# Performance work log

Measured on AMD Instinct MI355X. Metric: run time of the kernel, lower is better.

Reference implementation:

```python
import jax, jax.numpy as jnp
import numpy as np


def setup_inputs() -> dict:
    key = jax.random.key(0)
    ks = jax.random.split(key, 8)
    B, Cin, H, W = 4, 256, 64, 64
    Ck = Cin // 2            # 128, KAN in/out dim
    NC = 21                  # num_classes
    return {
        "x": jax.random.normal(ks[0], (B, Cin, H, W), dtype=jnp.float32),
        "conv1_w": jax.random.normal(ks[1], (Ck, Cin, 3, 3), dtype=jnp.float32) * 0.02,
        "conv1_b": jnp.zeros((Ck,), dtype=jnp.float32),
        "kan_scale": jnp.ones((Ck, Ck), dtype=jnp.float32)
                     + 0.1 * jax.random.normal(ks[2], (Ck, Ck), dtype=jnp.float32),
        "kan_translation": 0.1 * jax.random.normal(ks[3], (Ck, Ck), dtype=jnp.float32),
        "kan_wavelet_weight": jax.random.normal(ks[4], (Ck, Ck), dtype=jnp.float32) * 0.1,
        "kan_base_weight": jax.random.normal(ks[5], (Ck, Ck), dtype=jnp.float32) * 0.05,
        "conv2_w": jax.random.normal(ks[6], (NC, Ck, 1, 1), dtype=jnp.float32) * 0.05,
        "conv2_b": jnp.zeros((NC,), dtype=jnp.float32),
    }


def _conv2d(x, w, b, pad):
    y = jax.lax.conv_general_dilated(
        x, w, window_strides=(1, 1), padding=pad,
        dimension_numbers=("NCHW", "OIHW", "NCHW"))
    return y + b[None, :, None, None]


def _wavelet_kan(x, scale, translation, wav_w, base_w):
    # x: (N, Cin). Wav-KAN (DoG) layer:
    #   u = (x - translation) / scale, per (out, in) pair -> (N, O, I)
    #   dog(u) = -u * exp(-u^2 / 2)
    #   wavelet_out[n, o] = sum_i dog(u)[n, o, i] * wav_w[o, i]
    #   base_out = silu(x) @ base_w.T
    u = (x[:, None, :] - translation[None]) / scale[None]          # (N, O, I)
    dog = -u * jnp.exp(-0.5 * u * u)                               # (N, O, I)
    wav_out = jnp.einsum("noi,oi->no", dog, wav_w)                 # (N, O)
    base_out = jnp.einsum("ni,oi->no", jax.nn.silu(x), base_w)     # (N, O)
    return wav_out + base_out


def reference(x, conv1_w, conv1_b, kan_scale, kan_translation,
              kan_wavelet_weight, kan_base_weight, conv2_w, conv2_b):
    h = jax.nn.relu(_conv2d(x, conv1_w, conv1_b, ((1, 1), (1, 1))))   # (B, Ck, H, W)
    B, C, H, W = h.shape
    flat = h.transpose(0, 2, 3, 1).reshape(B * H * W, C)              # (N, Ck)
    k = _wavelet_kan(flat, kan_scale, kan_translation,
                     kan_wavelet_weight, kan_base_weight)             # (N, Ck)
    k = k.reshape(B, H, W, -1).transpose(0, 3, 1, 2)                  # (B, Ck, H, W)
    return _conv2d(k, conv2_w, conv2_b, ((0, 0), (0, 0)))             # (B, NC, H, W)
```

## Files before the change

### kernel.cpp

```cpp
#include <hip/hip_runtime.h>
#include <math.h>

typedef __attribute__((ext_vector_type(8))) short s16x8;
typedef __attribute__((ext_vector_type(4))) float f32x4;
typedef __attribute__((ext_vector_type(2))) float f32x2;

#define LOG2E 1.4426950408889634f

#define OFF_XH   0
#define OFF_WB   2097152
#define OFF_PQT  2244608
#define OFF_W2   2310144
#define OFF_H    2315520

__global__ __launch_bounds__(256) void transpose_x_k(
    const float* __restrict__ x, unsigned short* __restrict__ xh) {
  __shared__ float lsm[64][65];
  int blk = blockIdx.x;
  int pr = blk & 63, cib = (blk >> 6) & 3, bb = blk >> 8;
  int t = threadIdx.x;
  int sp0 = pr * 64;
  const float* src = x + (unsigned)(bb * 256 + cib * 64) * 4096 + sp0;
#pragma unroll
  for (int rr = 0; rr < 16; ++rr) {
    int idx = rr * 256 + t;
    int ci = idx >> 6, px = idx & 63;
    lsm[ci][px] = src[ci * 4096 + px];
  }
  __syncthreads();
#pragma unroll
  for (int rr = 0; rr < 16; ++rr) {
    int idx = rr * 256 + t;
    int px = idx >> 6, ci = idx & 63;
    unsigned u = __float_as_uint(lsm[ci][px]);
    xh[(unsigned)(bb * 4096 + sp0 + px) * 256 + cib * 64 + ci] =
        (unsigned short)((u + 0x7FFF + ((u >> 16) & 1)) >> 16);
  }
}

__global__ __launch_bounds__(256) void prep_w_k(
    const float* __restrict__ w1, const float* __restrict__ ks,
    const float* __restrict__ kt, const float* __restrict__ kw,
    const float* __restrict__ w2, float* __restrict__ ws) {
  int tid = blockIdx.x * 256 + threadIdx.x;
  unsigned short* Wb = (unsigned short*)(ws + OFF_WB);
  if (tid < 294912) {
    int j = tid & 7, co = (tid >> 3) & 63, g = (tid >> 9) & 3, r = tid >> 11;
    int t9 = r % 9, q = r / 9, ck = q & 7, chh = q >> 3;
    int ci = ck * 32 + g * 8 + j, cog = chh * 64 + co;
    unsigned u = __float_as_uint(w1[(unsigned)(cog * 256 + ci) * 9 + t9]);
    Wb[tid] = (unsigned short)((u + 0x7FFF + ((u >> 16) & 1)) >> 16);
  } else if (tid < 294912 + 16384) {
    int i2 = tid - 294912;
    int i = i2 >> 7, o = i2 & 127;
    int ic = i >> 3, k = i & 7;
    float rs = 1.f / ks[o * 128 + i];
    float T  = kt[o * 128 + i];
    float A  = -0.7213475204444817f * rs * rs;
    float Bq = -2.f * A * T;
    float C  = A * T * T;
    float P0 = -rs * kw[o * 128 + i];
    float sc = exp2f(C);
    int khi = k >> 2, klo = k & 3;
    unsigned base = ((unsigned)ic * 8 * 128 + o) * 4 + klo;
    ws[OFF_PQT + base + (0 + khi) * 512] = A;
    ws[OFF_PQT + base + (2 + khi) * 512] = Bq;
    ws[OFF_PQT + base + (4 + khi) * 512] = P0 * sc;
    ws[OFF_PQT + base + (6 + khi) * 512] = -P0 * T * sc;
  } else if (tid < 294912 + 16384 + 2688) {
    int i3 = tid - 294912 - 16384;
    int nc = i3 >> 7, k = i3 & 127;
    ws[OFF_W2 + nc * 256 + k] = w2[nc * 128 + k];
  }
}

__global__ __launch_bounds__(128) void w2b_k(
    const float* __restrict__ w2, const float* __restrict__ bw,
    float* __restrict__ w2c) {
  int nc = blockIdx.x, i = threadIdx.x;
  float acc = 0.f;
  for (int o = 0; o < 128; ++o)
    acc = fmaf(w2[nc * 128 + o], bw[o * 128 + i], acc);
  w2c[nc * 256 + 128 + i] = acc;
}

__global__ __launch_bounds__(256, 2) void conv1_mfma_k(
    const unsigned short* __restrict__ xh, const unsigned short* __restrict__ Wb,
    const float* __restrict__ b1, float* __restrict__ h) {
  __shared__ unsigned short Asm[3 * 66 * 40];
  __shared__ unsigned short Bsm[18432];
  int blk = blockIdx.x;
  int ch = blk & 1, y = (blk >> 1) & 63, bb = blk >> 7;
  int t = threadIdx.x;
  int wave = t >> 6, lane = t & 63;
  int wx = wave & 1, wn = wave >> 1;
  int l15 = lane & 15, lg = lane >> 4;

  if (t < 6) {
    int r = t >> 1, xl = (t & 1) * 65;
    float4 z = {0, 0, 0, 0};
    float4* p = (float4*)&Asm[(r * 66 + xl) * 40];
    p[0] = z; p[1] = z; p[2] = z; p[3] = z; p[4] = z;
  }

  f32x4 acc[2][2];
  f32x4 zz = {0.f, 0.f, 0.f, 0.f};
  acc[0][0] = zz; acc[0][1] = zz; acc[1][0] = zz; acc[1][1] = zz;

  int r_st = t >> 6, x_st = t & 63;
  int gy = y - 1 + r_st;
  bool arow = (r_st < 3);
  bool yok = arow & (gy >= 0) & (gy < 64);
  const unsigned short* asrc = xh + (unsigned)(bb * 4096 + gy * 64 + x_st) * 256;
  unsigned short* adst = &Asm[(r_st * 66 + x_st + 1) * 40];
  const unsigned short* bslab = Wb + ch * 8 * 18432;

  for (int ck = 0; ck < 8; ++ck) {
    float4 v0 = {0, 0, 0, 0}, v1 = v0, v2 = v0, v3 = v0;
    if (yok) {
      const float4* s = (const float4*)(asrc + ck * 32);
      v0 = s[0]; v1 = s[1]; v2 = s[2]; v3 = s[3];
    }
    if (arow) { float4* d = (float4*)adst; d[0] = v0; d[1] = v1; d[2] = v2; d[3] = v3; }
    {
      const float4* s = (const float4*)(bslab + ck * 18432);
      float4* d = (float4*)Bsm;
#pragma unroll
      for (int j = 0; j < 9; ++j) d[j * 256 + t] = s[j * 256 + t];
    }
    __syncthreads();
#pragma unroll
    for (int t9 = 0; t9 < 9; ++t9) {
      int ky = t9 / 3, kx = t9 % 3;
      s16x8 a[2], b[2];
      int abase = (ky * 66 + wx * 32 + l15 + kx) * 40 + lg * 8;
#pragma unroll
      for (int f = 0; f < 2; ++f)
        a[f] = *(const s16x8*)&Asm[abase + f * 640];
#pragma unroll
      for (int n = 0; n < 2; ++n)
        b[n] = *(const s16x8*)&Bsm[((t9 * 4 + lg) * 64 + wn * 32 + n * 16 + l15) * 8];
#pragma unroll
      for (int f = 0; f < 2; ++f)
#pragma unroll
        for (int n = 0; n < 2; ++n)
          acc[f][n] = __builtin_amdgcn_mfma_f32_16x16x32_bf16(a[f], b[n], acc[f][n], 0, 0, 0);
    }
    __syncthreads();
  }
#pragma unroll
  for (int n = 0; n < 2; ++n) {
    int co = ch * 64 + wn * 32 + n * 16 + l15;
    float bz = b1[co];
#pragma unroll
    for (int f = 0; f < 2; ++f) {
      int xbase = wx * 32 + f * 16 + lg * 4;
      float* dst = h + (unsigned)(bb * 4096 + y * 64 + xbase) * 128 + co;
#pragma unroll
      for (int r = 0; r < 4; ++r) {
        float v = acc[f][n][r] + bz;
        dst[r * 128] = v > 0.f ? v : 0.f;
      }
    }
  }
}

__global__ __launch_bounds__(512) void wavkan_k(
    const float* __restrict__ h, const float* __restrict__ PQT,
    float* __restrict__ kwout) {
  __shared__ float hsm[16][128];
  __shared__ f32x2 red[4][8][64];
  int n0 = blockIdx.x * 16;
  int t = threadIdx.x;
  {
    int row = t >> 5, c4 = (t & 31) * 4;
    *(float4*)&hsm[row][c4] = *(const float4*)&h[(unsigned)(n0 + row) * 128 + c4];
  }
  __syncthreads();

  int wave = t >> 6, lane = t & 63;
  int ich = wave & 1;
  int oh  = (wave >> 1) & 1;
  int ng  = wave >> 2;
  int w2i = wave >> 1;
  int o  = oh * 64 + lane;
  int nb = ng * 8;

  f32x2 accv[8];
#pragma unroll
  for (int n = 0; n < 8; ++n) accv[n] = (f32x2){0.f, 0.f};

  const float4* pq = (const float4*)PQT + o;

  for (int ic = ich * 8; ic < ich * 8 + 8; ++ic) {
    const float4* pp = pq + (unsigned)ic * 1024;
    float4 r0 = pp[0],   r1 = pp[128], r2 = pp[256], r3 = pp[384],
           r4 = pp[512], r5 = pp[640], r6 = pp[768], r7 = pp[896];
    f32x2 A2[4] = {{r0.x, r0.y}, {r0.z, r0.w}, {r1.x, r1.y}, {r1.z, r1.w}};
    f32x2 B2[4] = {{r2.x, r2.y}, {r2.z, r2.w}, {r3.x, r3.y}, {r3.z, r3.w}};
    f32x2 P2[4] = {{r4.x, r4.y}, {r4.z, r4.w}, {r5.x, r5.y}, {r5.z, r5.w}};
    f32x2 D2[4] = {{r6.x, r6.y}, {r6.z, r6.w}, {r7.x, r7.y}, {r7.z, r7.w}};
    int i0 = ic * 8;
#pragma unroll
    for (int n = 0; n < 8; ++n) {
      float4 h0 = *(const float4*)&hsm[nb + n][i0];
      float4 h1 = *(const float4*)&hsm[nb + n][i0 + 4];
      f32x2 hh[4] = {{h0.x, h0.y}, {h0.z, h0.w}, {h1.x, h1.y}, {h1.z, h1.w}};
      f32x2 a2 = accv[n];
#pragma unroll
      for (int q = 0; q < 4; ++q) {
        f32x2 h2 = hh[q];
        f32x2 t2 = A2[q] * h2 + B2[q];
        f32x2 u2 = t2 * h2;
        f32x2 e2;
        e2.x = __builtin_amdgcn_exp2f(u2.x);
        e2.y = __builtin_amdgcn_exp2f(u2.y);
        f32x2 v2 = P2[q] * h2 + D2[q];
        a2 = v2 * e2 + a2;
      }
      accv[n] = a2;
    }
  }

  if (ich) {
#pragma unroll
    for (int n = 0; n < 8; ++n) red[w2i][n][lane] = accv[n];
  }
  __syncthreads();
  if (!ich) {
#pragma unroll
    for (int n = 0; n < 8; ++n) {
      f32x2 r = red[w2i][n][lane];
      kwout[(unsigned)(n0 + nb + n) * 128 + o] =
          (accv[n].x + r.x) + (accv[n].y + r.y);
    }
  }
}

__global__ __launch_bounds__(256) void conv2_k(
    const float* __restrict__ kwv, const float* __restrict__ h,
    const float* __restrict__ w2c, const float* __restrict__ b2,
    float* __restrict__ out) {
  __shared__ float ksm[32][260];
  __shared__ float wsm[21 * 256];
  int n0 = blockIdx.x * 32;
  int t = threadIdx.x;
#pragma unroll 2
  for (int rr = 0; rr < 4; ++rr) {
    int idx4 = rr * 256 + t;
    int row = idx4 >> 5, c4 = (idx4 & 31) * 4;
    *(float4*)&ksm[row][c4] = *(const float4*)&kwv[(unsigned)(n0 + row) * 128 + c4];
    float4 v = *(const float4*)&h[(unsigned)(n0 + row) * 128 + c4];
    float4 s;
    s.x = v.x * __builtin_amdgcn_rcpf(1.f + __builtin_amdgcn_exp2f(-LOG2E * v.x));
    s.y = v.y * __builtin_amdgcn_rcpf(1.f + __builtin_amdgcn_exp2f(-LOG2E * v.y));
    s.z = v.z * __builtin_amdgcn_rcpf(1.f + __builtin_amdgcn_exp2f(-LOG2E * v.z));
    s.w = v.w * __builtin_amdgcn_rcpf(1.f + __builtin_amdgcn_exp2f(-LOG2E * v.w));
    *(float4*)&ksm[row][128 + c4] = s;
  }
#pragma unroll 2
  for (int j = t; j < 1344; j += 256)
    *(float4*)&wsm[j * 4] = *(const float4*)&w2c[j * 4];
  __syncthreads();

  int n = t & 31, ncg = t >> 5;
  float a0 = 0.f, a1 = 0.f, a2 = 0.f;
  bool has2 = ncg < 5;
#pragma unroll 4
  for (int i4 = 0; i4 < 64; ++i4) {
    float4 k4 = *(const float4*)&ksm[n][i4 * 4];
    float4 wA = *(const float4*)&wsm[ncg * 256 + i4 * 4];
    float4 wB = *(const float4*)&wsm[(ncg + 8) * 256 + i4 * 4];
    a0 += k4.x * wA.x + k4.y * wA.y + k4.z * wA.z + k4.w * wA.w;
    a1 += k4.x * wB.x + k4.y * wB.y + k4.z * wB.z + k4.w * wB.w;
    if (has2) {
      float4 wC = *(const float4*)&wsm[(ncg + 16) * 256 + i4 * 4];
      a2 += k4.x * wC.x + k4.y * wC.y + k4.z * wC.z + k4.w * wC.w;
    }
  }
  int gn = n0 + n, bb = gn >> 12, sp = gn & 4095;
  out[(unsigned)(bb * 21 + ncg) * 4096 + sp] = a0 + b2[ncg];
  out[(unsigned)(bb * 21 + ncg + 8) * 4096 + sp] = a1 + b2[ncg + 8];
  if (has2) out[(unsigned)(bb * 21 + ncg + 16) * 4096 + sp] = a2 + b2[ncg + 16];
}

extern "C" void kernel_launch(void* const* d_in, const int* in_sizes, int n_in,
                              void* d_out, int out_size, void* d_ws, size_t ws_size,
                              hipStream_t stream) {
  const float* x  = (const float*)d_in[0];
  const float* w1 = (const float*)d_in[1];
  const float* b1 = (const float*)d_in[2];
  const float* ks = (const float*)d_in[3];
  const float* kt = (const float*)d_in[4];
  const float* kw = (const float*)d_in[5];
  const float* kb = (const float*)d_in[6];
  const float* w2 = (const float*)d_in[7];
  const float* b2 = (const float*)d_in[8];
  float* out = (float*)d_out;
  float* ws  = (float*)d_ws;

  transpose_x_k<<<1024, 256, 0, stream>>>(x, (unsigned short*)(ws + OFF_XH));
  prep_w_k<<<1227, 256, 0, stream>>>(w1, ks, kt, kw, w2, ws);
  w2b_k<<<21, 128, 0, stream>>>(w2, kb, ws + OFF_W2);
  conv1_mfma_k<<<512, 256, 0, stream>>>((const unsigned short*)(ws + OFF_XH),
                                        (const unsigned short*)(ws + OFF_WB),
                                        b1, ws + OFF_H);
  wavkan_k<<<1024, 512, 0, stream>>>(ws + OFF_H, ws + OFF_PQT,
                                     ws + OFF_XH );
  conv2_k<<<512, 256, 0, stream>>>(ws + OFF_XH, ws + OFF_H, ws + OFF_W2, b2, out);
}
```

Measured before the change: 96.01 us.

## Stage KAN params through double-buffered LDS and drop split-K reduction in wavkan

The wavkan kernel now has each block cooperatively load every 16 KB chunk of precomputed KAN parameters into a double-buffered shared-memory tile, prefetching the next chunk into registers while computing. Before, each wave read parameters straight from global memory. The work split also changes: each wave now covers all 128 inputs for 4 rows instead of half the inputs for 8 rows, so the cross-wave reduction through shared memory goes away. The goal is less redundant global/L2 traffic for parameters, at the price of two barriers per input chunk and more LDS use.

```diff
diff --git a/kernel.cpp b/kernel.cpp
--- a/kernel.cpp
+++ b/kernel.cpp
@@ -169,40 +169,45 @@
     const float* __restrict__ h, const float* __restrict__ PQT,
     float* __restrict__ kwout) {
   __shared__ float hsm[16][128];
-  __shared__ f32x2 red[4][8][64];
+  __shared__ float4 psm[2][1024];
   int n0 = blockIdx.x * 16;
   int t = threadIdx.x;
   {
     int row = t >> 5, c4 = (t & 31) * 4;
     *(float4*)&hsm[row][c4] = *(const float4*)&h[(unsigned)(n0 + row) * 128 + c4];
   }
-  __syncthreads();
-
   int wave = t >> 6, lane = t & 63;
-  int ich = wave & 1;
-  int oh  = (wave >> 1) & 1;
-  int ng  = wave >> 2;
-  int w2i = wave >> 1;
+  int oh = wave & 1;
+  int ng = wave >> 1;
   int o  = oh * 64 + lane;
-  int nb = ng * 8;
-
-  f32x2 accv[8];
-#pragma unroll
-  for (int n = 0; n < 8; ++n) accv[n] = (f32x2){0.f, 0.f};
-
-  const float4* pq = (const float4*)PQT + o;
-
-  for (int ic = ich * 8; ic < ich * 8 + 8; ++ic) {
-    const float4* pp = pq + (unsigned)ic * 1024;
-    float4 r0 = pp[0],   r1 = pp[128], r2 = pp[256], r3 = pp[384],
-           r4 = pp[512], r5 = pp[640], r6 = pp[768], r7 = pp[896];
+  int nb = ng * 4;
+
+  f32x2 accv[4];
+#pragma unroll
+  for (int n = 0; n < 4; ++n) accv[n] = (f32x2){0.f, 0.f};
+
+  const float4* pqg = (const float4*)PQT;
+  float4 s0 = pqg[t * 2], s1 = pqg[t * 2 + 1];
+
+  for (int ic = 0; ic < 16; ++ic) {
+    int cur = ic & 1;
+    psm[cur][t * 2] = s0;
+    psm[cur][t * 2 + 1] = s1;
+    if (ic < 15) {
+      s0 = pqg[(unsigned)(ic + 1) * 1024 + t * 2];
+      s1 = pqg[(unsigned)(ic + 1) * 1024 + t * 2 + 1];
+    }
+    __syncthreads();
+    const float4* pb = &psm[cur][o];
+    float4 r0 = pb[0],   r1 = pb[128], r2 = pb[256], r3 = pb[384],
+           r4 = pb[512], r5 = pb[640], r6 = pb[768], r7 = pb[896];
     f32x2 A2[4] = {{r0.x, r0.y}, {r0.z, r0.w}, {r1.x, r1.y}, {r1.z, r1.w}};
     f32x2 B2[4] = {{r2.x, r2.y}, {r2.z, r2.w}, {r3.x, r3.y}, {r3.z, r3.w}};
     f32x2 P2[4] = {{r4.x, r4.y}, {r4.z, r4.w}, {r5.x, r5.y}, {r5.z, r5.w}};
     f32x2 D2[4] = {{r6.x, r6.y}, {r6.z, r6.w}, {r7.x, r7.y}, {r7.z, r7.w}};
     int i0 = ic * 8;
 #pragma unroll
-    for (int n = 0; n < 8; ++n) {
+    for (int n = 0; n < 4; ++n) {
       float4 h0 = *(const float4*)&hsm[nb + n][i0];
       float4 h1 = *(const float4*)&hsm[nb + n][i0 + 4];
       f32x2 hh[4] = {{h0.x, h0.y}, {h0.z, h0.w}, {h1.x, h1.y}, {h1.z, h1.w}};
@@ -220,21 +225,11 @@
       }
       accv[n] = a2;
     }
-  }
-
-  if (ich) {
-#pragma unroll
-    for (int n = 0; n < 8; ++n) red[w2i][n][lane] = accv[n];
-  }
-  __syncthreads();
-  if (!ich) {
-#pragma unroll
-    for (int n = 0; n < 8; ++n) {
-      f32x2 r = red[w2i][n][lane];
-      kwout[(unsigned)(n0 + nb + n) * 128 + o] =
-          (accv[n].x + r.x) + (accv[n].y + r.y);
-    }
-  }
+    __syncthreads();
+  }
+#pragma unroll
+  for (int n = 0; n < 4; ++n)
+    kwout[(unsigned)(n0 + nb + n) * 128 + o] = accv[n].x + accv[n].y;
 }
 
 __global__ __launch_bounds__(256) void conv2_k(
```

After: 97.55 us. No clear change (+1.6%).
